# Kernel tuning notes

Measured on AMD Instinct MI355X. Metric: run time of the kernel, lower is better.

## Reference

```python
import jax, jax.numpy as jnp
import numpy as np

N = 100000     # nodes
E = 1600000    # edges
H = 64         # hidden_channels
FIN = 4        # input feature dim (GraphNorm(4))
EPS = 1e-5
STEPS = 3      # Set2Set processing steps


def setup_inputs() -> dict:
    key = jax.random.key(0)
    ks = jax.random.split(key, 20)
    rn = lambda k, shape, s=1.0: jax.random.normal(k, shape, dtype=jnp.float32) * s

    def gn_params(k, d):
        k1, k2 = jax.random.split(k)
        return (1.0 + 0.1 * rn(k1, (d,)), 0.1 * rn(k2, (d,)), jnp.ones((d,), jnp.float32))

    inp = {}
    inp['x'] = rn(ks[0], (N, FIN))
    inp['gn0_w'], inp['gn0_b'], inp['gn0_ms'] = gn_params(ks[1], FIN)
    inp['W1'] = rn(ks[2], (FIN, H), 1.0 / np.sqrt(FIN))
    inp['b1'] = 0.01 * rn(ks[3], (H,))
    inp['a1'] = 0.25 * jnp.ones((H,), jnp.float32)
    inp['gn1_w'], inp['gn1_b'], inp['gn1_ms'] = gn_params(ks[4], H)
    inp['W2'] = rn(ks[5], (H, H), 1.0 / np.sqrt(H))
    inp['b2'] = 0.01 * rn(ks[6], (H,))
    inp['a2'] = 0.25 * jnp.ones((H,), jnp.float32)
    inp['gn2_w'], inp['gn2_b'], inp['gn2_ms'] = gn_params(ks[7], H)
    inp['W3'] = rn(ks[8], (H, H), 1.0 / np.sqrt(H))
    inp['b3'] = 0.01 * rn(ks[9], (H,))
    inp['gn3_w'], inp['gn3_b'], inp['gn3_ms'] = gn_params(ks[10], H)
    s = 1.0 / np.sqrt(H)
    inp['Wih'] = rn(ks[11], (4 * H, 2 * H), s)  # LSTM input weights, gate order i,f,g,o
    inp['Whh'] = rn(ks[12], (4 * H, H), s)
    inp['bih'] = rn(ks[13], (4 * H,), s)
    inp['bhh'] = rn(ks[14], (4 * H,), s)
    inp['edge_index'] = jax.random.randint(ks[15], (2, E), 0, N, dtype=jnp.int32)
    return inp


def _graph_norm(x, w, b, ms):
    # single graph (batch all zeros): per-feature mean/var over all nodes
    mean = x.mean(0)
    out = x - ms * mean
    var = (out * out).mean(0)
    return w * out / jnp.sqrt(var + EPS) + b


def _prelu(x, a):
    return jnp.where(x >= 0, x, a * x)


def _gcn(x, W, b, src, dst, dinv):
    # GCNConv: D^{-1/2} (A + I) D^{-1/2} X W + b
    xw = x @ W
    coef = dinv[src] * dinv[dst]
    agg = jax.ops.segment_sum(xw[src] * coef[:, None], dst, num_segments=N)
    agg = agg + xw * (dinv * dinv)[:, None]  # self-loop contribution
    return agg + b


def reference(x, gn0_w, gn0_b, gn0_ms, W1, b1, a1, gn1_w, gn1_b, gn1_ms,
              W2, b2, a2, gn2_w, gn2_b, gn2_ms, W3, b3, gn3_w, gn3_b, gn3_ms,
              Wih, Whh, bih, bhh, edge_index):
    src, dst = edge_index[0], edge_index[1]
    deg = jax.ops.segment_sum(jnp.ones((E,), jnp.float32), dst, num_segments=N) + 1.0
    dinv = 1.0 / jnp.sqrt(deg)

    h = _graph_norm(x, gn0_w, gn0_b, gn0_ms)
    h = _prelu(_gcn(h, W1, b1, src, dst, dinv), a1)
    h = _graph_norm(h, gn1_w, gn1_b, gn1_ms)
    h = _prelu(_gcn(h, W2, b2, src, dst, dinv), a2)
    h = _graph_norm(h, gn2_w, gn2_b, gn2_ms)
    h = _gcn(h, W3, b3, src, dst, dinv)
    h = _graph_norm(h, gn3_w, gn3_b, gn3_ms)

    # Set2Set pooling over a single graph (batch forced to zeros in forward)
    q_star = jnp.zeros((1, 2 * H), jnp.float32)
    hs = jnp.zeros((1, H), jnp.float32)
    c = jnp.zeros((1, H), jnp.float32)
    for _ in range(STEPS):
        gates = q_star @ Wih.T + bih + hs @ Whh.T + bhh
        i, f, g, o = jnp.split(gates, 4, axis=-1)
        c = jax.nn.sigmoid(f) * c + jax.nn.sigmoid(i) * jnp.tanh(g)
        hs = jax.nn.sigmoid(o) * jnp.tanh(c)
        e = h @ hs[0]                    # [N] attention logits
        a = jax.nn.softmax(e)
        r = (a[:, None] * h).sum(0, keepdims=True)  # [1, H] readout
        q_star = jnp.concatenate([hs, r], axis=-1)
    return q_star  # [1, 2H]
```

## Files before the change

kernel.cpp:

```cpp
#include <hip/hip_runtime.h>

#define NN 100000
#define NE 1600000
#define HID 64
#define EPSV 1e-5f
#define NB_ATT 256

#define NBUK 391
#define BCAP 4608
#define BTILE 4096
#define NTILES 391

#define SM_SUMS(l)  ((l)*128)
#define SM_SUMSQ(l) ((l)*128 + 64)
#define SM_HS       512
#define SM_C        576
#define SM_HV       768
#define SM_EOFF     832
#define SM_COUNT    1024

#define NPAD        100352L
#define OFF_DINV    1024L
#define OFF_H       (OFF_DINV + NPAD)
#define OFF_Y32     (OFF_H + 6400000L)
#define OFF_PART    (OFF_Y32 + 3200000L)
#define OFF_INT     (OFF_PART + 69632L)

static __device__ __forceinline__ unsigned bf16rne(float f) {
  unsigned u = __float_as_uint(f);
  return (u + 0x7fffu + ((u >> 16) & 1u)) >> 16;
}
static __device__ __forceinline__ unsigned packbf2(float lo, float hi) {
  return bf16rne(lo) | (bf16rne(hi) << 16);
}
static __device__ __forceinline__ float bflo(unsigned w) { return __uint_as_float(w << 16); }
static __device__ __forceinline__ float bfhi(unsigned w) { return __uint_as_float(w & 0xffff0000u); }

static __device__ __forceinline__ void gn_affine(int j, const float* w, const float* b,
                                                 const float* ms, const float* sums,
                                                 const float* sumsq, float& sc, float& sh) {
  const float invn = 1.0f / (float)NN;
  float mean = sums[j] * invn;
  float ex2  = sumsq[j] * invn;
  float m    = ms[j];
  float var  = ex2 - m * mean * mean * (2.0f - m);
  sc = w[j] * rsqrtf(var + EPSV);
  sh = b[j] - sc * m * mean;
}

__global__ __launch_bounds__(512) void k_binit(int* __restrict__ gcursor) {
  int t = threadIdx.x;
  if (t < NBUK) gcursor[t] = t * BCAP;
}

__global__ __launch_bounds__(256) void k_bin(const int* __restrict__ src, const int* __restrict__ dst,
                                             int* __restrict__ gcursor, unsigned* __restrict__ stage) {
  __shared__ int hist[NBUK], base[NBUK];
  int t = threadIdx.x;
  long tile0 = (long)blockIdx.x * BTILE;
  for (int b = t; b < NBUK; b += 256) hist[b] = 0;
  __syncthreads();
  unsigned v[16]; int bk[16];
#pragma unroll
  for (int k = 0; k < 16; ++k) {
    long e = tile0 + k * 256 + t;
    if (e < NE) {
      int d = dst[e], s = src[e];
      bk[k] = d >> 8;
      v[k] = ((unsigned)(d & 255) << 24) | (unsigned)s;
      atomicAdd(&hist[bk[k]], 1);
    } else bk[k] = -1;
  }
  __syncthreads();
  for (int b = t; b < NBUK; b += 256) {
    int c = hist[b];
    base[b] = c ? atomicAdd(&gcursor[b], c) : 0;
    hist[b] = 0;
  }
  __syncthreads();
#pragma unroll
  for (int k = 0; k < 16; ++k) {
    if (bk[k] >= 0) {
      int off = atomicAdd(&hist[bk[k]], 1);
      stage[base[bk[k]] + off] = v[k];
    }
  }
}

__global__ __launch_bounds__(512) void k_bscan(const int* __restrict__ gcursor,
                                               int* __restrict__ boff, int* __restrict__ rowptr) {
  __shared__ int ws[8];
  int t = threadIdx.x, lane = t & 63;
  int c = (t < NBUK) ? (gcursor[t] - t * BCAP) : 0;
  int incl = c;
#pragma unroll
  for (int off = 1; off < 64; off <<= 1) {
    int u = __shfl_up(incl, off, 64);
    if (lane >= off) incl += u;
  }
  if (lane == 63) ws[t >> 6] = incl;
  __syncthreads();
  if (t == 0) {
    int s = 0;
#pragma unroll
    for (int w = 0; w < 8; ++w) { int tv = ws[w]; ws[w] = s; s += tv; }
  }
  __syncthreads();
  if (t < NBUK) boff[t] = incl - c + ws[t >> 6];
  if (t == 0) { boff[NBUK] = NE; rowptr[NN] = NE; }
}

__global__ __launch_bounds__(256) void k_bsort(const unsigned* __restrict__ stage,
                                               const int* __restrict__ boff,
                                               int* __restrict__ col, int* __restrict__ rowptr,
                                               float* __restrict__ dinv) {
  __shared__ int hist[256], cur[256];
  __shared__ int ws[4];
  int b = blockIdx.x;
  int t = threadIdx.x, lane = t & 63;
  int sb = b * BCAP;
  int b0 = boff[b], cb = boff[b + 1] - b0;
  hist[t] = 0;
  __syncthreads();
  for (int j = t; j < cb; j += 256)
    atomicAdd(&hist[stage[sb + j] >> 24], 1);
  __syncthreads();
  int c = hist[t];
  int incl = c;
#pragma unroll
  for (int off = 1; off < 64; off <<= 1) {
    int u = __shfl_up(incl, off, 64);
    if (lane >= off) incl += u;
  }
  if (lane == 63) ws[t >> 6] = incl;
  __syncthreads();
  int woff = 0;
  if (t >= 64) woff += ws[0];
  if (t >= 128) woff += ws[1];
  if (t >= 192) woff += ws[2];
  int gbase = b0 + (incl - c) + woff;
  int node = b * 256 + t;
  if (node < NN) {
    rowptr[node] = gbase;
    dinv[node] = rsqrtf((float)c + 1.0f);
  }
  cur[t] = gbase;
  __syncthreads();
  for (int j = t; j < cb; j += 256) {
    unsigned v = stage[sb + j];
    int pos = atomicAdd(&cur[v >> 24], 1);
    col[pos] = (int)(v & 0xffffffu);
  }
}

__global__ __launch_bounds__(256) void k_sums4(const float* __restrict__ x,
                                               float* __restrict__ sums, float* __restrict__ sumsq) {
  __shared__ float ls[256], lq[256];
  int t = threadIdx.x;
  float s = 0.f, q = 0.f;
  int stride = gridDim.x * blockDim.x;
  for (int idx = blockIdx.x * blockDim.x + t; idx < NN * 4; idx += stride) {
    float v = x[idx];
    s += v; q += v * v;
  }
  ls[t] = s; lq[t] = q;
  __syncthreads();
  if (t < 4) {
    float S = 0.f, Q = 0.f;
    for (int g = t; g < 256; g += 4) { S += ls[g]; Q += lq[g]; }
    atomicAdd(&sums[t], S);
    atomicAdd(&sumsq[t], Q);
  }
}

template <int D>
__global__ __launch_bounds__(256) void k_mm(const float* __restrict__ hin, const float* __restrict__ W,
                                            const float* __restrict__ gw, const float* __restrict__ gb,
                                            const float* __restrict__ gms,
                                            const float* __restrict__ sums, const float* __restrict__ sumsq,
                                            const float* __restrict__ dinv,
                                            unsigned* __restrict__ y32) {
  __shared__ float4 Ws4[D][16];
  __shared__ float4 woff4[16];
  __shared__ float scale[D], shift[D];
  __shared__ float hl[16][68];
  int t = threadIdx.x;
  if (t < D) {
    float sc, sh;
    gn_affine(t, gw, gb, gms, sums, sumsq, sc, sh);
    scale[t] = sc; shift[t] = sh;
  }
  __syncthreads();
  for (int idx = t; idx < D * 64; idx += 256) {
    int k = idx >> 6;
    ((float*)Ws4)[idx] = scale[k] * W[idx];
  }
  __syncthreads();
  if (t < 64) {
    float o = 0.f;
#pragma unroll
    for (int k = 0; k < D; ++k) o += shift[k] * W[k * 64 + t];
    ((float*)woff4)[t] = o;
  }
  __syncthreads();

  int row = t >> 4, cg = t & 15;
  const int nG = NN / 16;
  for (int g = blockIdx.x; g < nG; g += gridDim.x) {
    if (D == 64) {
      *(float4*)&hl[row][cg * 4] = *(const float4*)(hin + (long)(g * 16 + row) * 64 + cg * 4);
    } else {
      if (t < 64) hl[t >> 2][t & 3] = hin[g * 64 + t];
    }
    __syncthreads();
    float4 acc = woff4[cg];
#pragma unroll
    for (int k = 0; k < D; ++k) {
      float hk = hl[row][k];
      float4 w4 = Ws4[k][cg];
      acc.x += hk * w4.x; acc.y += hk * w4.y;
      acc.z += hk * w4.z; acc.w += hk * w4.w;
    }
    int node = g * 16 + row;
    float di = dinv[node];
    uint2 u;
    u.x = packbf2(di * acc.x, di * acc.y);
    u.y = packbf2(di * acc.z, di * acc.w);
    *(uint2*)(y32 + (long)node * 32 + 2 * cg) = u;
    __syncthreads();
  }
}

#define ACC4(W) { f[0]+=bflo(W.x); f[1]+=bfhi(W.x); f[2]+=bflo(W.y); f[3]+=bfhi(W.y); \
                  f[4]+=bflo(W.z); f[5]+=bfhi(W.z); f[6]+=bflo(W.w); f[7]+=bfhi(W.w); }

template <bool PR, bool HB>
__global__ __launch_bounds__(256) void k_gather_fin(const uint4* __restrict__ y4,
                                                    const int* __restrict__ rowptr, const int* __restrict__ col,
                                                    const float* __restrict__ dinv,
                                                    const float* __restrict__ b, const float* __restrict__ a,
                                                    float* __restrict__ h, uint4* __restrict__ hb4,
                                                    float* __restrict__ sums, float* __restrict__ sumsq) {
  __shared__ float lsum[4][64], lsq[4][64];
  int t = threadIdx.x, lane = t & 63, w = t >> 6;
  int o = lane >> 3, l7 = lane & 7;
  float bv[8], av[8];
#pragma unroll
  for (int k = 0; k < 8; ++k) {
    bv[k] = b[8 * l7 + k];
    av[k] = PR ? a[8 * l7 + k] : 1.f;
  }
  float sa[8] = {0,0,0,0,0,0,0,0}, qa[8] = {0,0,0,0,0,0,0,0};
  int nwaves = gridDim.x * 4;
  for (int i = blockIdx.x * 4 + w; i < NN; i += nwaves) {
    float f[8] = {0,0,0,0,0,0,0,0};
    int p = rowptr[i], p1 = rowptr[i + 1];
    for (; p + 16 <= p1; p += 16) {
      int c0 = col[p + o], c1 = col[p + 8 + o];
      uint4 wa = y4[c0 * 8 + l7];
      uint4 wb = y4[c1 * 8 + l7];
      ACC4(wa); ACC4(wb);
    }
    if (p + 8 <= p1) {
      int c0 = col[p + o];
      uint4 wa = y4[c0 * 8 + l7];
      ACC4(wa);
      p += 8;
    }
    {
      int r = p1 - p;
      int c = (o < r) ? col[p + o] : ((o == r) ? i : -1);
      if (c >= 0) {
        uint4 wa = y4[c * 8 + l7];
        ACC4(wa);
      }
    }
#pragma unroll
    for (int k = 0; k < 8; ++k) {
      float v = f[k];
      v += __shfl_xor(v, 8, 64);
      v += __shfl_xor(v, 16, 64);
      v += __shfl_xor(v, 32, 64);
      f[k] = v;
    }
    float di = dinv[i];
    float vo[8];
#pragma unroll
    for (int k = 0; k < 8; ++k) {
      float v = di * f[k] + bv[k];
      if (PR && v < 0.f) v *= av[k];
      vo[k] = v;
      sa[k] += v; qa[k] += v * v;
    }
    if (o == 0) {
      if (HB) {
        uint4 u;
        u.x = packbf2(vo[0], vo[1]); u.y = packbf2(vo[2], vo[3]);
        u.z = packbf2(vo[4], vo[5]); u.w = packbf2(vo[6], vo[7]);
        hb4[(long)i * 8 + l7] = u;
      } else {
        *(float4*)(h + (long)i * 64 + 8 * l7)     = make_float4(vo[0], vo[1], vo[2], vo[3]);
        *(float4*)(h + (long)i * 64 + 8 * l7 + 4) = make_float4(vo[4], vo[5], vo[6], vo[7]);
      }
    }
  }
  if (o == 0) {
#pragma unroll
    for (int k = 0; k < 8; ++k) { lsum[w][8 * l7 + k] = sa[k]; lsq[w][8 * l7 + k] = qa[k]; }
  }
  __syncthreads();
  if (t < 64) {
    float S = lsum[0][t] + lsum[1][t] + lsum[2][t] + lsum[3][t];
    float Q = lsq[0][t] + lsq[1][t] + lsq[2][t] + lsq[3][t];
    atomicAdd(&sums[t], S);
    atomicAdd(&sumsq[t], Q);
  }
}

__global__ __launch_bounds__(256) void k_att(const uint4* __restrict__ hb4, const float* __restrict__ sm,
                                             float* __restrict__ part) {
  __shared__ float gm[32], gz[32], gr[32][64];
  int t = threadIdx.x;
  int grp = t >> 3, l7 = t & 7;
  float hvr[8];
#pragma unroll
  for (int k = 0; k < 8; ++k) hvr[k] = sm[SM_HV + 8 * l7 + k];
  float eoff = sm[SM_EOFF];
  float m = -3.4e38f, z = 0.f;
  float r[8] = {0,0,0,0,0,0,0,0};
  int ngrp = gridDim.x * 32;
  for (int i = blockIdx.x * 32 + grp; i < NN; i += ngrp) {
    uint4 hw = hb4[(long)i * 8 + l7];
    float hx[8] = { bflo(hw.x), bfhi(hw.x), bflo(hw.y), bfhi(hw.y),
                    bflo(hw.z), bfhi(hw.z), bflo(hw.w), bfhi(hw.w) };
    float dot = 0.f;
#pragma unroll
    for (int k = 0; k < 8; ++k) dot += hx[k] * hvr[k];
    dot += __shfl_xor(dot, 1, 64);
    dot += __shfl_xor(dot, 2, 64);
    dot += __shfl_xor(dot, 4, 64);
    float e = dot + eoff;
    float mn = fmaxf(m, e);
    float sa = expf(m - mn);
    float pb = expf(e - mn);
    z = z * sa + pb;
#pragma unroll
    for (int k = 0; k < 8; ++k) r[k] = r[k] * sa + pb * hx[k];
    m = mn;
  }
#pragma unroll
  for (int k = 0; k < 8; ++k) gr[grp][8 * l7 + k] = r[k];
  if (l7 == 0) { gm[grp] = m; gz[grp] = z; }
  __syncthreads();
  if (t < 64) {
    float mb = gm[0];
#pragma unroll
    for (int k = 1; k < 32; ++k) mb = fmaxf(mb, gm[k]);
    float rb = 0.f, zb = 0.f;
#pragma unroll 8
    for (int k = 0; k < 32; ++k) {
      float scl = expf(gm[k] - mb);
      rb += gr[k][t] * scl;
      zb += gz[k] * scl;
    }
    part[blockIdx.x * 68 + t] = rb;
    if (t == 0) { part[blockIdx.x * 68 + 64] = mb; part[blockIdx.x * 68 + 65] = zb; }
  }
}

__global__ __launch_bounds__(256) void k_attfin(const float* __restrict__ part,
                                                const float* __restrict__ gw, const float* __restrict__ gb,
                                                const float* __restrict__ gms,
                                                const float* __restrict__ sums, const float* __restrict__ sumsq,
                                                const float* __restrict__ Wih, const float* __restrict__ Whh,
                                                const float* __restrict__ bih, const float* __restrict__ bhh,
                                                float* __restrict__ sm, float* __restrict__ out, int mode) {
  __shared__ float hsL[64], cL[64], qsL[128], gL[256], red[256], sf[NB_ATT], rr4[4][64];
  int t = threadIdx.x, lane = t & 63, w = t >> 6;
  if (t < 64) { hsL[t] = sm[SM_HS + t]; cL[t] = sm[SM_C + t]; }
  __syncthreads();
  if (mode > 0) {
    float mv = part[t * 68 + 64];
    red[t] = mv; __syncthreads();
    for (int s = 128; s; s >>= 1) { if (t < s) red[t] = fmaxf(red[t], red[t + s]); __syncthreads(); }
    float mg = red[0];
    __syncthreads();
    float sc_ = expf(mv - mg);
    sf[t] = sc_;
    red[t] = part[t * 68 + 65] * sc_; __syncthreads();
    for (int s = 128; s; s >>= 1) { if (t < s) red[t] += red[t + s]; __syncthreads(); }
    float zg = red[0];
    __syncthreads();
    float racc = 0.f;
#pragma unroll 8
    for (int j = 0; j < 64; ++j) {
      int bk = 4 * j + w;
      racc += part[bk * 68 + lane] * sf[bk];
    }
    rr4[w][lane] = racc;
    __syncthreads();
    if (t < 64) {
      float rg = rr4[0][t] + rr4[1][t] + rr4[2][t] + rr4[3][t];
      float sc, sh;
      gn_affine(t, gw, gb, gms, sums, sumsq, sc, sh);
      float rr = sc * (rg / zg) + sh;
      qsL[t] = hsL[t]; qsL[64 + t] = rr;
      if (mode == 2) { out[t] = hsL[t]; out[64 + t] = rr; }
    }
  } else {
    if (t < 64) { qsL[t] = 0.f; qsL[64 + t] = 0.f; hsL[t] = 0.f; cL[t] = 0.f; }
  }
  __syncthreads();
  if (mode == 2) return;
  float g = bih[t] + bhh[t];
#pragma unroll 16
  for (int k = 0; k < 128; ++k) g += qsL[k] * Wih[t * 128 + k];
#pragma unroll 16
  for (int k = 0; k < 64; ++k) g += hsL[k] * Whh[t * 64 + k];
  gL[t] = g;
  __syncthreads();
  if (t < 64) {
    float ig = 1.f / (1.f + expf(-gL[t]));
    float fg = 1.f / (1.f + expf(-gL[64 + t]));
    float gg = tanhf(gL[128 + t]);
    float og = 1.f / (1.f + expf(-gL[192 + t]));
    float c = fg * cL[t] + ig * gg;
    float hsn = og * tanhf(c);
    sm[SM_C + t] = c;
    sm[SM_HS + t] = hsn;
    float sc, sh;
    gn_affine(t, gw, gb, gms, sums, sumsq, sc, sh);
    sm[SM_HV + t] = sc * hsn;
    red[t] = sh * hsn;
  }
  __syncthreads();
  if (t == 0) {
    float s = 0.f;
    for (int k = 0; k < 64; ++k) s += red[k];
    sm[SM_EOFF] = s;
  }
}

extern "C" void kernel_launch(void* const* d_in, const int* in_sizes, int n_in,
                              void* d_out, int out_size, void* d_ws, size_t ws_size,
                              hipStream_t stream) {
  const float* x     = (const float*)d_in[0];
  const float* gn0_w = (const float*)d_in[1];
  const float* gn0_b = (const float*)d_in[2];
  const float* gn0_ms= (const float*)d_in[3];
  const float* W1    = (const float*)d_in[4];
  const float* b1    = (const float*)d_in[5];
  const float* a1    = (const float*)d_in[6];
  const float* gn1_w = (const float*)d_in[7];
  const float* gn1_b = (const float*)d_in[8];
  const float* gn1_ms= (const float*)d_in[9];
  const float* W2    = (const float*)d_in[10];
  const float* b2    = (const float*)d_in[11];
  const float* a2    = (const float*)d_in[12];
  const float* gn2_w = (const float*)d_in[13];
  const float* gn2_b = (const float*)d_in[14];
  const float* gn2_ms= (const float*)d_in[15];
  const float* W3    = (const float*)d_in[16];
  const float* b3    = (const float*)d_in[17];
  const float* gn3_w = (const float*)d_in[18];
  const float* gn3_b = (const float*)d_in[19];
  const float* gn3_ms= (const float*)d_in[20];
  const float* Wih   = (const float*)d_in[21];
  const float* Whh   = (const float*)d_in[22];
  const float* bih   = (const float*)d_in[23];
  const float* bhh   = (const float*)d_in[24];
  const int*   eidx  = (const int*)d_in[25];
  const int* esrc = eidx;
  const int* edst = eidx + NE;

  float* sm   = (float*)d_ws;
  float* dinv = sm + OFF_DINV;
  float* h    = sm + OFF_H;
  unsigned* stage = (unsigned*)(sm + OFF_H);
  uint4* hb4  = (uint4*)(sm + OFF_H);
  unsigned* y32 = (unsigned*)(sm + OFF_Y32);
  const uint4* y4 = (const uint4*)y32;
  float* part = sm + OFF_PART;
  int* col    = (int*)(sm + OFF_INT);
  int* rowptr = col + NE;
  int* gcursor= rowptr + NPAD;
  int* boff   = gcursor + 512;
  float* out  = (float*)d_out;

  hipMemsetAsync(sm, 0, SM_COUNT * sizeof(float), stream);

  k_binit<<<1, 512, 0, stream>>>(gcursor);
  k_bin<<<NTILES, 256, 0, stream>>>(esrc, edst, gcursor, stage);
  k_bscan<<<1, 512, 0, stream>>>(gcursor, boff, rowptr);
  k_bsort<<<NBUK, 256, 0, stream>>>(stage, boff, col, rowptr, dinv);

  k_sums4<<<1024, 256, 0, stream>>>(x, sm + SM_SUMS(0), sm + SM_SUMSQ(0));

  k_mm<4><<<1024, 256, 0, stream>>>(x, W1, gn0_w, gn0_b, gn0_ms,
                                    sm + SM_SUMS(0), sm + SM_SUMSQ(0), dinv, y32);
  k_gather_fin<true, false><<<2048, 256, 0, stream>>>(y4, rowptr, col, dinv, b1, a1, h, nullptr,
                                                      sm + SM_SUMS(1), sm + SM_SUMSQ(1));
  k_mm<64><<<1024, 256, 0, stream>>>(h, W2, gn1_w, gn1_b, gn1_ms,
                                     sm + SM_SUMS(1), sm + SM_SUMSQ(1), dinv, y32);
  k_gather_fin<true, false><<<2048, 256, 0, stream>>>(y4, rowptr, col, dinv, b2, a2, h, nullptr,
                                                      sm + SM_SUMS(2), sm + SM_SUMSQ(2));
  k_mm<64><<<1024, 256, 0, stream>>>(h, W3, gn2_w, gn2_b, gn2_ms,
                                     sm + SM_SUMS(2), sm + SM_SUMSQ(2), dinv, y32);
  k_gather_fin<false, true><<<2048, 256, 0, stream>>>(y4, rowptr, col, dinv, b3, nullptr, nullptr, hb4,
                                                      sm + SM_SUMS(3), sm + SM_SUMSQ(3));

  k_attfin<<<1, 256, 0, stream>>>(part, gn3_w, gn3_b, gn3_ms,
                                  sm + SM_SUMS(3), sm + SM_SUMSQ(3),
                                  Wih, Whh, bih, bhh, sm, nullptr, 0);
  for (int s = 0; s < 3; ++s) {
    k_att<<<NB_ATT, 256, 0, stream>>>(hb4, sm, part);
    k_attfin<<<1, 256, 0, stream>>>(part, gn3_w, gn3_b, gn3_ms,
                                    sm + SM_SUMS(3), sm + SM_SUMSQ(3),
                                    Wih, Whh, bih, bhh, sm,
                                    (s == 2) ? out : nullptr, (s == 2) ? 2 : 1);
  }
}
```

Measured before the change: 455.8 us.

## Fuse graph build and Set2Set tail into persistent kernels with grid barriers

Merges the binning, bucket scan, bucket sort and input-stat kernels into one persistent k_build kernel separated by software grid barriers, and merges the seven attention/LSTM tail launches into one k_tail kernel that also uses grid barriers. It also prefetches the next node's rowptr in the gather loop. The intent is to remove many small kernel launches and their gaps. The risk is that the spin barriers depend on all 784 or 256 blocks being resident at once, and that barrier latency may cost more than the launches it replaces.

```diff
diff --git a/kernel.cpp b/kernel.cpp
--- a/kernel.cpp
+++ b/kernel.cpp
@@ -8,8 +8,9 @@
 
 #define NBUK 391
 #define BCAP 4608
-#define BTILE 4096
-#define NTILES 391
+#define BTILE 2048
+#define NTILES 782
+#define NB_BUILD 784
 
 #define SM_SUMS(l)  ((l)*128)
 #define SM_SUMSQ(l) ((l)*128 + 64)
@@ -17,10 +18,12 @@
 #define SM_C        576
 #define SM_HV       768
 #define SM_EOFF     832
-#define SM_COUNT    1024
+#define SM_BAR      960
+#define SM_GCUR     1024
+#define SM_ZEND     1424
 
 #define NPAD        100352L
-#define OFF_DINV    1024L
+#define OFF_DINV    1424L
 #define OFF_H       (OFF_DINV + NPAD)
 #define OFF_Y32     (OFF_H + 6400000L)
 #define OFF_PART    (OFF_Y32 + 3200000L)
@@ -48,128 +51,156 @@
   sh = b[j] - sc * m * mean;
 }
 
-__global__ __launch_bounds__(512) void k_binit(int* __restrict__ gcursor) {
-  int t = threadIdx.x;
-  if (t < NBUK) gcursor[t] = t * BCAP;
-}
-
-__global__ __launch_bounds__(256) void k_bin(const int* __restrict__ src, const int* __restrict__ dst,
-                                             int* __restrict__ gcursor, unsigned* __restrict__ stage) {
+static __device__ __forceinline__ void gridbar(int* cnt, unsigned* flag, int nb) {
+  __syncthreads();
+  if (threadIdx.x == 0) {
+    __threadfence();
+    unsigned gen = atomicAdd(flag, 0u);
+    if (atomicAdd(cnt, 1) == nb - 1) {
+      atomicExch(cnt, 0);
+      __threadfence();
+      atomicAdd(flag, 1u);
+    } else {
+      while (atomicAdd(flag, 0u) == gen) __builtin_amdgcn_s_sleep(1);
+    }
+    __threadfence();
+  }
+  __syncthreads();
+}
+
+__global__ __launch_bounds__(256, 4) void k_build(const int* __restrict__ src, const int* __restrict__ dst,
+                                                  const float* __restrict__ x,
+                                                  int* __restrict__ gcursor, unsigned* __restrict__ stage,
+                                                  int* __restrict__ boff,
+                                                  int* __restrict__ col, int* __restrict__ rowptr,
+                                                  float* __restrict__ dinv,
+                                                  float* __restrict__ sums0, float* __restrict__ sumsq0,
+                                                  int* __restrict__ barc, unsigned* __restrict__ barf) {
   __shared__ int hist[NBUK], base[NBUK];
-  int t = threadIdx.x;
-  long tile0 = (long)blockIdx.x * BTILE;
-  for (int b = t; b < NBUK; b += 256) hist[b] = 0;
-  __syncthreads();
-  unsigned v[16]; int bk[16];
-#pragma unroll
-  for (int k = 0; k < 16; ++k) {
-    long e = tile0 + k * 256 + t;
-    if (e < NE) {
-      int d = dst[e], s = src[e];
-      bk[k] = d >> 8;
-      v[k] = ((unsigned)(d & 255) << 24) | (unsigned)s;
-      atomicAdd(&hist[bk[k]], 1);
-    } else bk[k] = -1;
-  }
-  __syncthreads();
-  for (int b = t; b < NBUK; b += 256) {
-    int c = hist[b];
-    base[b] = c ? atomicAdd(&gcursor[b], c) : 0;
-    hist[b] = 0;
-  }
-  __syncthreads();
-#pragma unroll
-  for (int k = 0; k < 16; ++k) {
-    if (bk[k] >= 0) {
-      int off = atomicAdd(&hist[bk[k]], 1);
-      stage[base[bk[k]] + off] = v[k];
-    }
-  }
-}
-
-__global__ __launch_bounds__(512) void k_bscan(const int* __restrict__ gcursor,
-                                               int* __restrict__ boff, int* __restrict__ rowptr) {
+  __shared__ int hist256[256], cur256[256];
   __shared__ int ws[8];
   int t = threadIdx.x, lane = t & 63;
-  int c = (t < NBUK) ? (gcursor[t] - t * BCAP) : 0;
-  int incl = c;
-#pragma unroll
-  for (int off = 1; off < 64; off <<= 1) {
-    int u = __shfl_up(incl, off, 64);
-    if (lane >= off) incl += u;
-  }
-  if (lane == 63) ws[t >> 6] = incl;
-  __syncthreads();
-  if (t == 0) {
-    int s = 0;
-#pragma unroll
-    for (int w = 0; w < 8; ++w) { int tv = ws[w]; ws[w] = s; s += tv; }
-  }
-  __syncthreads();
-  if (t < NBUK) boff[t] = incl - c + ws[t >> 6];
-  if (t == 0) { boff[NBUK] = NE; rowptr[NN] = NE; }
-}
-
-__global__ __launch_bounds__(256) void k_bsort(const unsigned* __restrict__ stage,
-                                               const int* __restrict__ boff,
-                                               int* __restrict__ col, int* __restrict__ rowptr,
-                                               float* __restrict__ dinv) {
-  __shared__ int hist[256], cur[256];
-  __shared__ int ws[4];
-  int b = blockIdx.x;
-  int t = threadIdx.x, lane = t & 63;
-  int sb = b * BCAP;
-  int b0 = boff[b], cb = boff[b + 1] - b0;
-  hist[t] = 0;
-  __syncthreads();
-  for (int j = t; j < cb; j += 256)
-    atomicAdd(&hist[stage[sb + j] >> 24], 1);
-  __syncthreads();
-  int c = hist[t];
-  int incl = c;
-#pragma unroll
-  for (int off = 1; off < 64; off <<= 1) {
-    int u = __shfl_up(incl, off, 64);
-    if (lane >= off) incl += u;
-  }
-  if (lane == 63) ws[t >> 6] = incl;
-  __syncthreads();
-  int woff = 0;
-  if (t >= 64) woff += ws[0];
-  if (t >= 128) woff += ws[1];
-  if (t >= 192) woff += ws[2];
-  int gbase = b0 + (incl - c) + woff;
-  int node = b * 256 + t;
-  if (node < NN) {
-    rowptr[node] = gbase;
-    dinv[node] = rsqrtf((float)c + 1.0f);
-  }
-  cur[t] = gbase;
-  __syncthreads();
-  for (int j = t; j < cb; j += 256) {
-    unsigned v = stage[sb + j];
-    int pos = atomicAdd(&cur[v >> 24], 1);
-    col[pos] = (int)(v & 0xffffffu);
-  }
-}
-
-__global__ __launch_bounds__(256) void k_sums4(const float* __restrict__ x,
-                                               float* __restrict__ sums, float* __restrict__ sumsq) {
-  __shared__ float ls[256], lq[256];
-  int t = threadIdx.x;
-  float s = 0.f, q = 0.f;
-  int stride = gridDim.x * blockDim.x;
-  for (int idx = blockIdx.x * blockDim.x + t; idx < NN * 4; idx += stride) {
-    float v = x[idx];
-    s += v; q += v * v;
-  }
-  ls[t] = s; lq[t] = q;
-  __syncthreads();
-  if (t < 4) {
-    float S = 0.f, Q = 0.f;
-    for (int g = t; g < 256; g += 4) { S += ls[g]; Q += lq[g]; }
-    atomicAdd(&sums[t], S);
-    atomicAdd(&sumsq[t], Q);
+
+  for (int tile = blockIdx.x; tile < NTILES; tile += gridDim.x) {
+    __syncthreads();
+    for (int b = t; b < NBUK; b += 256) hist[b] = 0;
+    __syncthreads();
+    long e0 = (long)tile * BTILE;
+    unsigned v[8]; int bk[8];
+#pragma unroll
+    for (int k = 0; k < 8; ++k) {
+      long e = e0 + k * 256 + t;
+      if (e < NE) {
+        int d = dst[e], s = src[e];
+        bk[k] = d >> 8;
+        v[k] = ((unsigned)(d & 255) << 24) | (unsigned)s;
+        atomicAdd(&hist[bk[k]], 1);
+      } else bk[k] = -1;
+    }
+    __syncthreads();
+    for (int b = t; b < NBUK; b += 256) {
+      int c = hist[b];
+      base[b] = c ? atomicAdd(&gcursor[b], c) : 0;
+      hist[b] = 0;
+    }
+    __syncthreads();
+#pragma unroll
+    for (int k = 0; k < 8; ++k) {
+      if (bk[k] >= 0) {
+        int bkk = bk[k];
+        int off = atomicAdd(&hist[bkk], 1);
+        stage[(long)bkk * BCAP + base[bkk] + off] = v[k];
+      }
+    }
+  }
+
+  {
+    const float4* x4 = (const float4*)x;
+    float4 s4 = make_float4(0.f, 0.f, 0.f, 0.f);
+    float4 q4 = make_float4(0.f, 0.f, 0.f, 0.f);
+    int stride = gridDim.x * 256;
+    for (int i = blockIdx.x * 256 + t; i < NN; i += stride) {
+      float4 xv = x4[i];
+      s4.x += xv.x; s4.y += xv.y; s4.z += xv.z; s4.w += xv.w;
+      q4.x += xv.x * xv.x; q4.y += xv.y * xv.y; q4.z += xv.z * xv.z; q4.w += xv.w * xv.w;
+    }
+#pragma unroll
+    for (int off = 32; off; off >>= 1) {
+      s4.x += __shfl_xor(s4.x, off, 64); s4.y += __shfl_xor(s4.y, off, 64);
+      s4.z += __shfl_xor(s4.z, off, 64); s4.w += __shfl_xor(s4.w, off, 64);
+      q4.x += __shfl_xor(q4.x, off, 64); q4.y += __shfl_xor(q4.y, off, 64);
+      q4.z += __shfl_xor(q4.z, off, 64); q4.w += __shfl_xor(q4.w, off, 64);
+    }
+    if (lane == 0) {
+      atomicAdd(&sums0[0], s4.x); atomicAdd(&sums0[1], s4.y);
+      atomicAdd(&sums0[2], s4.z); atomicAdd(&sums0[3], s4.w);
+      atomicAdd(&sumsq0[0], q4.x); atomicAdd(&sumsq0[1], q4.y);
+      atomicAdd(&sumsq0[2], q4.z); atomicAdd(&sumsq0[3], q4.w);
+    }
+  }
+
+  gridbar(barc, barf, gridDim.x);
+
+  if (blockIdx.x == 0) {
+    int t2 = 2 * t;
+    int c0 = (t2 < NBUK) ? gcursor[t2] : 0;
+    int c1 = (t2 + 1 < NBUK) ? gcursor[t2 + 1] : 0;
+    int ls = c0 + c1;
+    int incl = ls;
+#pragma unroll
+    for (int off = 1; off < 64; off <<= 1) {
+      int u = __shfl_up(incl, off, 64);
+      if (lane >= off) incl += u;
+    }
+    if (lane == 63) ws[t >> 6] = incl;
+    __syncthreads();
+    int woff = 0;
+    if (t >= 64) woff += ws[0];
+    if (t >= 128) woff += ws[1];
+    if (t >= 192) woff += ws[2];
+    int excl = incl - ls + woff;
+    if (t2 < NBUK) boff[t2] = excl;
+    if (t2 + 1 < NBUK) boff[t2 + 1] = excl + c0;
+    if (t == 0) { boff[NBUK] = NE; rowptr[NN] = NE; }
+  }
+
+  gridbar(barc, barf, gridDim.x);
+
+  for (int b = blockIdx.x; b < NBUK; b += gridDim.x) {
+    __syncthreads();
+    long sb = (long)b * BCAP;
+    int b0 = boff[b], cb = boff[b + 1] - b0;
+    hist256[t] = 0;
+    __syncthreads();
+    for (int j = t; j < cb; j += 256)
+      atomicAdd(&hist256[stage[sb + j] >> 24], 1);
+    __syncthreads();
+    int c = hist256[t];
+    int incl = c;
+#pragma unroll
+    for (int off = 1; off < 64; off <<= 1) {
+      int u = __shfl_up(incl, off, 64);
+      if (lane >= off) incl += u;
+    }
+    if (lane == 63) ws[t >> 6] = incl;
+    __syncthreads();
+    int woff = 0;
+    if (t >= 64) woff += ws[0];
+    if (t >= 128) woff += ws[1];
+    if (t >= 192) woff += ws[2];
+    int gbase = b0 + (incl - c) + woff;
+    int node = b * 256 + t;
+    if (node < NN) {
+      rowptr[node] = gbase;
+      dinv[node] = rsqrtf((float)c + 1.0f);
+    }
+    cur256[t] = gbase;
+    __syncthreads();
+    for (int j = t; j < cb; j += 256) {
+      unsigned v = stage[sb + j];
+      int pos = atomicAdd(&cur256[v >> 24], 1);
+      col[pos] = (int)(v & 0xffffffu);
+    }
   }
 }
 
@@ -252,9 +283,14 @@
   }
   float sa[8] = {0,0,0,0,0,0,0,0}, qa[8] = {0,0,0,0,0,0,0,0};
   int nwaves = gridDim.x * 4;
-  for (int i = blockIdx.x * 4 + w; i < NN; i += nwaves) {
+  int i = blockIdx.x * 4 + w;
+  int p = 0, p1 = 0;
+  if (i < NN) { p = rowptr[i]; p1 = rowptr[i + 1]; }
+  while (i < NN) {
+    int inext = i + nwaves;
+    int pn = 0, pn1 = 0;
+    if (inext < NN) { pn = rowptr[inext]; pn1 = rowptr[inext + 1]; }
     float f[8] = {0,0,0,0,0,0,0,0};
-    int p = rowptr[i], p1 = rowptr[i + 1];
     for (; p + 16 <= p1; p += 16) {
       int c0 = col[p + o], c1 = col[p + 8 + o];
       uint4 wa = y4[c0 * 8 + l7];
@@ -303,6 +339,7 @@
         *(float4*)(h + (long)i * 64 + 8 * l7 + 4) = make_float4(vo[4], vo[5], vo[6], vo[7]);
       }
     }
+    i = inext; p = pn; p1 = pn1;
   }
   if (o == 0) {
 #pragma unroll
@@ -317,9 +354,13 @@
   }
 }
 
-__global__ __launch_bounds__(256) void k_att(const uint4* __restrict__ hb4, const float* __restrict__ sm,
-                                             float* __restrict__ part) {
-  __shared__ float gm[32], gz[32], gr[32][64];
+struct TailSmem {
+  float gm[32], gz[32], gr[32][64];
+  float hsL[64], cL[64], qsL[128], gL[256], red[256], sf[NB_ATT], rr4[4][64];
+};
+
+static __device__ void att_phase(TailSmem& S, const uint4* __restrict__ hb4,
+                                 const float* __restrict__ sm, float* __restrict__ part) {
   int t = threadIdx.x;
   int grp = t >> 3, l7 = t & 7;
   float hvr[8];
@@ -341,103 +382,125 @@
     dot += __shfl_xor(dot, 4, 64);
     float e = dot + eoff;
     float mn = fmaxf(m, e);
-    float sa = expf(m - mn);
+    float sc = expf(m - mn);
     float pb = expf(e - mn);
-    z = z * sa + pb;
-#pragma unroll
-    for (int k = 0; k < 8; ++k) r[k] = r[k] * sa + pb * hx[k];
+    z = z * sc + pb;
+#pragma unroll
+    for (int k = 0; k < 8; ++k) r[k] = r[k] * sc + pb * hx[k];
     m = mn;
   }
 #pragma unroll
-  for (int k = 0; k < 8; ++k) gr[grp][8 * l7 + k] = r[k];
-  if (l7 == 0) { gm[grp] = m; gz[grp] = z; }
+  for (int k = 0; k < 8; ++k) S.gr[grp][8 * l7 + k] = r[k];
+  if (l7 == 0) { S.gm[grp] = m; S.gz[grp] = z; }
   __syncthreads();
   if (t < 64) {
-    float mb = gm[0];
-#pragma unroll
-    for (int k = 1; k < 32; ++k) mb = fmaxf(mb, gm[k]);
+    float mb = S.gm[0];
+#pragma unroll
+    for (int k = 1; k < 32; ++k) mb = fmaxf(mb, S.gm[k]);
     float rb = 0.f, zb = 0.f;
 #pragma unroll 8
     for (int k = 0; k < 32; ++k) {
-      float scl = expf(gm[k] - mb);
-      rb += gr[k][t] * scl;
-      zb += gz[k] * scl;
+      float scl = expf(S.gm[k] - mb);
+      rb += S.gr[k][t] * scl;
+      zb += S.gz[k] * scl;
     }
     part[blockIdx.x * 68 + t] = rb;
     if (t == 0) { part[blockIdx.x * 68 + 64] = mb; part[blockIdx.x * 68 + 65] = zb; }
   }
-}
-
-__global__ __launch_bounds__(256) void k_attfin(const float* __restrict__ part,
-                                                const float* __restrict__ gw, const float* __restrict__ gb,
-                                                const float* __restrict__ gms,
-                                                const float* __restrict__ sums, const float* __restrict__ sumsq,
-                                                const float* __restrict__ Wih, const float* __restrict__ Whh,
-                                                const float* __restrict__ bih, const float* __restrict__ bhh,
-                                                float* __restrict__ sm, float* __restrict__ out, int mode) {
-  __shared__ float hsL[64], cL[64], qsL[128], gL[256], red[256], sf[NB_ATT], rr4[4][64];
+  __syncthreads();
+}
+
+static __device__ void fin_phase(TailSmem& S, const float* __restrict__ part,
+                                 const float* __restrict__ gw, const float* __restrict__ gb,
+                                 const float* __restrict__ gms,
+                                 const float* __restrict__ sums, const float* __restrict__ sumsq,
+                                 const float* __restrict__ Wih, const float* __restrict__ Whh,
+                                 const float* __restrict__ bih, const float* __restrict__ bhh,
+                                 float* __restrict__ sm, float* __restrict__ out, int mode) {
   int t = threadIdx.x, lane = t & 63, w = t >> 6;
-  if (t < 64) { hsL[t] = sm[SM_HS + t]; cL[t] = sm[SM_C + t]; }
+  if (t < 64) { S.hsL[t] = sm[SM_HS + t]; S.cL[t] = sm[SM_C + t]; }
   __syncthreads();
   if (mode > 0) {
     float mv = part[t * 68 + 64];
-    red[t] = mv; __syncthreads();
-    for (int s = 128; s; s >>= 1) { if (t < s) red[t] = fmaxf(red[t], red[t + s]); __syncthreads(); }
-    float mg = red[0];
+    S.red[t] = mv; __syncthreads();
+    for (int s = 128; s; s >>= 1) { if (t < s) S.red[t] = fmaxf(S.red[t], S.red[t + s]); __syncthreads(); }
+    float mg = S.red[0];
     __syncthreads();
     float sc_ = expf(mv - mg);
-    sf[t] = sc_;
-    red[t] = part[t * 68 + 65] * sc_; __syncthreads();
-    for (int s = 128; s; s >>= 1) { if (t < s) red[t] += red[t + s]; __syncthreads(); }
-    float zg = red[0];
+    S.sf[t] = sc_;
+    S.red[t] = part[t * 68 + 65] * sc_; __syncthreads();
+    for (int s = 128; s; s >>= 1) { if (t < s) S.red[t] += S.red[t + s]; __syncthreads(); }
+    float zg = S.red[0];
     __syncthreads();
     float racc = 0.f;
 #pragma unroll 8
     for (int j = 0; j < 64; ++j) {
       int bk = 4 * j + w;
-      racc += part[bk * 68 + lane] * sf[bk];
-    }
-    rr4[w][lane] = racc;
+      racc += part[bk * 68 + lane] * S.sf[bk];
+    }
+    S.rr4[w][lane] = racc;
     __syncthreads();
     if (t < 64) {
-      float rg = rr4[0][t] + rr4[1][t] + rr4[2][t] + rr4[3][t];
+      float rg = S.rr4[0][t] + S.rr4[1][t] + S.rr4[2][t] + S.rr4[3][t];
       float sc, sh;
       gn_affine(t, gw, gb, gms, sums, sumsq, sc, sh);
       float rr = sc * (rg / zg) + sh;
-      qsL[t] = hsL[t]; qsL[64 + t] = rr;
-      if (mode == 2) { out[t] = hsL[t]; out[64 + t] = rr; }
+      S.qsL[t] = S.hsL[t]; S.qsL[64 + t] = rr;
+      if (mode == 2) { out[t] = S.hsL[t]; out[64 + t] = rr; }
     }
   } else {
-    if (t < 64) { qsL[t] = 0.f; qsL[64 + t] = 0.f; hsL[t] = 0.f; cL[t] = 0.f; }
+    if (t < 64) { S.qsL[t] = 0.f; S.qsL[64 + t] = 0.f; S.hsL[t] = 0.f; S.cL[t] = 0.f; }
   }
   __syncthreads();
   if (mode == 2) return;
   float g = bih[t] + bhh[t];
 #pragma unroll 16
-  for (int k = 0; k < 128; ++k) g += qsL[k] * Wih[t * 128 + k];
+  for (int k = 0; k < 128; ++k) g += S.qsL[k] * Wih[t * 128 + k];
 #pragma unroll 16
-  for (int k = 0; k < 64; ++k) g += hsL[k] * Whh[t * 64 + k];
-  gL[t] = g;
+  for (int k = 0; k < 64; ++k) g += S.hsL[k] * Whh[t * 64 + k];
+  S.gL[t] = g;
   __syncthreads();
   if (t < 64) {
-    float ig = 1.f / (1.f + expf(-gL[t]));
-    float fg = 1.f / (1.f + expf(-gL[64 + t]));
-    float gg = tanhf(gL[128 + t]);
-    float og = 1.f / (1.f + expf(-gL[192 + t]));
-    float c = fg * cL[t] + ig * gg;
+    float ig = 1.f / (1.f + expf(-S.gL[t]));
+    float fg = 1.f / (1.f + expf(-S.gL[64 + t]));
+    float gg = tanhf(S.gL[128 + t]);
+    float og = 1.f / (1.f + expf(-S.gL[192 + t]));
+    float c = fg * S.cL[t] + ig * gg;
     float hsn = og * tanhf(c);
     sm[SM_C + t] = c;
     sm[SM_HS + t] = hsn;
     float sc, sh;
     gn_affine(t, gw, gb, gms, sums, sumsq, sc, sh);
     sm[SM_HV + t] = sc * hsn;
-    red[t] = sh * hsn;
+    S.red[t] = sh * hsn;
   }
   __syncthreads();
   if (t == 0) {
     float s = 0.f;
-    for (int k = 0; k < 64; ++k) s += red[k];
+    for (int k = 0; k < 64; ++k) s += S.red[k];
     sm[SM_EOFF] = s;
+  }
+  __syncthreads();
+}
+
+__global__ __launch_bounds__(256) void k_tail(const uint4* __restrict__ hb4, float* __restrict__ part,
+                                              const float* __restrict__ gw, const float* __restrict__ gb,
+                                              const float* __restrict__ gms,
+                                              const float* __restrict__ sums, const float* __restrict__ sumsq,
+                                              const float* __restrict__ Wih, const float* __restrict__ Whh,
+                                              const float* __restrict__ bih, const float* __restrict__ bhh,
+                                              float* __restrict__ sm, float* __restrict__ out,
+                                              int* __restrict__ barc, unsigned* __restrict__ barf) {
+  __shared__ TailSmem S;
+  if (blockIdx.x == 0)
+    fin_phase(S, part, gw, gb, gms, sums, sumsq, Wih, Whh, bih, bhh, sm, nullptr, 0);
+  for (int s = 0; s < 3; ++s) {
+    gridbar(barc, barf, gridDim.x);
+    att_phase(S, hb4, sm, part);
+    gridbar(barc, barf, gridDim.x);
+    if (blockIdx.x == 0)
+      fin_phase(S, part, gw, gb, gms, sums, sumsq, Wih, Whh, bih, bhh, sm,
+                (s == 2) ? out : nullptr, (s == 2) ? 2 : 1);
   }
 }
 
@@ -474,6 +537,11 @@
   const int* edst = eidx + NE;
 
   float* sm   = (float*)d_ws;
+  int* gcursor= (int*)(sm + SM_GCUR);
+  int* barc   = (int*)(sm + SM_BAR);
+  unsigned* barf = (unsigned*)(sm + SM_BAR + 1);
+  int* barc2  = (int*)(sm + SM_BAR + 2);
+  unsigned* barf2 = (unsigned*)(sm + SM_BAR + 3);
   float* dinv = sm + OFF_DINV;
   float* h    = sm + OFF_H;
   unsigned* stage = (unsigned*)(sm + OFF_H);
@@ -483,18 +551,13 @@
   float* part = sm + OFF_PART;
   int* col    = (int*)(sm + OFF_INT);
   int* rowptr = col + NE;
-  int* gcursor= rowptr + NPAD;
-  int* boff   = gcursor + 512;
+  int* boff   = rowptr + NPAD;
   float* out  = (float*)d_out;
 
-  hipMemsetAsync(sm, 0, SM_COUNT * sizeof(float), stream);
-
-  k_binit<<<1, 512, 0, stream>>>(gcursor);
-  k_bin<<<NTILES, 256, 0, stream>>>(esrc, edst, gcursor, stage);
-  k_bscan<<<1, 512, 0, stream>>>(gcursor, boff, rowptr);
-  k_bsort<<<NBUK, 256, 0, stream>>>(stage, boff, col, rowptr, dinv);
-
-  k_sums4<<<1024, 256, 0, stream>>>(x, sm + SM_SUMS(0), sm + SM_SUMSQ(0));
+  hipMemsetAsync(sm, 0, SM_ZEND * sizeof(float), stream);
+
+  k_build<<<NB_BUILD, 256, 0, stream>>>(esrc, edst, x, gcursor, stage, boff, col, rowptr, dinv,
+                                        sm + SM_SUMS(0), sm + SM_SUMSQ(0), barc, barf);
 
   k_mm<4><<<1024, 256, 0, stream>>>(x, W1, gn0_w, gn0_b, gn0_ms,
                                     sm + SM_SUMS(0), sm + SM_SUMSQ(0), dinv, y32);
@@ -509,14 +572,7 @@
   k_gather_fin<false, true><<<2048, 256, 0, stream>>>(y4, rowptr, col, dinv, b3, nullptr, nullptr, hb4,
                                                       sm + SM_SUMS(3), sm + SM_SUMSQ(3));
 
-  k_attfin<<<1, 256, 0, stream>>>(part, gn3_w, gn3_b, gn3_ms,
-                                  sm + SM_SUMS(3), sm + SM_SUMSQ(3),
-                                  Wih, Whh, bih, bhh, sm, nullptr, 0);
-  for (int s = 0; s < 3; ++s) {
-    k_att<<<NB_ATT, 256, 0, stream>>>(hb4, sm, part);
-    k_attfin<<<1, 256, 0, stream>>>(part, gn3_w, gn3_b, gn3_ms,
-                                    sm + SM_SUMS(3), sm + SM_SUMSQ(3),
-                                    Wih, Whh, bih, bhh, sm,
-                                    (s == 2) ? out : nullptr, (s == 2) ? 2 : 1);
-  }
-}
+  k_tail<<<NB_ATT, 256, 0, stream>>>(hb4, part, gn3_w, gn3_b, gn3_ms,
+                                     sm + SM_SUMS(3), sm + SM_SUMSQ(3),
+                                     Wih, Whh, bih, bhh, sm, out, barc2, barf2);
+}
```

Result: slower. 846.6 us (+85.7%).

## Slice gather by feature chunk per block, fuse input stats into binning

Applied to the files above, without the earlier changes.

Each gather block now handles one 16-byte feature slice (blockIdx&7) across groups of 8 nodes, with 8 lanes striding edges per node. The intent is to shrink the per-pass working set of the gathered feature table so it fits better in cache. The x mean/variance reduction is folded into the binning kernel and the bucket-cursor init kernel is replaced by a memset, cutting two launches. Costs: rowptr and col are re-read by all 8 slices, and load balance is worse when node degrees vary.

```diff
diff --git a/kernel.cpp b/kernel.cpp
--- a/kernel.cpp
+++ b/kernel.cpp
@@ -5,6 +5,7 @@
 #define HID 64
 #define EPSV 1e-5f
 #define NB_ATT 256
+#define NGRP 12500
 
 #define NBUK 391
 #define BCAP 4608
@@ -17,10 +18,11 @@
 #define SM_C        576
 #define SM_HV       768
 #define SM_EOFF     832
-#define SM_COUNT    1024
+#define SM_GCUR     1024
+#define SM_ZEND     1424
 
 #define NPAD        100352L
-#define OFF_DINV    1024L
+#define OFF_DINV    1424L
 #define OFF_H       (OFF_DINV + NPAD)
 #define OFF_Y32     (OFF_H + 6400000L)
 #define OFF_PART    (OFF_Y32 + 3200000L)
@@ -48,15 +50,12 @@
   sh = b[j] - sc * m * mean;
 }
 
-__global__ __launch_bounds__(512) void k_binit(int* __restrict__ gcursor) {
-  int t = threadIdx.x;
-  if (t < NBUK) gcursor[t] = t * BCAP;
-}
-
 __global__ __launch_bounds__(256) void k_bin(const int* __restrict__ src, const int* __restrict__ dst,
-                                             int* __restrict__ gcursor, unsigned* __restrict__ stage) {
+                                             const float* __restrict__ x,
+                                             int* __restrict__ gcursor, unsigned* __restrict__ stage,
+                                             float* __restrict__ sums0, float* __restrict__ sumsq0) {
   __shared__ int hist[NBUK], base[NBUK];
-  int t = threadIdx.x;
+  int t = threadIdx.x, lane = t & 63;
   long tile0 = (long)blockIdx.x * BTILE;
   for (int b = t; b < NBUK; b += 256) hist[b] = 0;
   __syncthreads();
@@ -81,9 +80,32 @@
 #pragma unroll
   for (int k = 0; k < 16; ++k) {
     if (bk[k] >= 0) {
-      int off = atomicAdd(&hist[bk[k]], 1);
-      stage[base[bk[k]] + off] = v[k];
-    }
+      int bkk = bk[k];
+      int off = atomicAdd(&hist[bkk], 1);
+      stage[(long)bkk * BCAP + base[bkk] + off] = v[k];
+    }
+  }
+  const float4* x4 = (const float4*)x;
+  float4 s4 = make_float4(0.f, 0.f, 0.f, 0.f);
+  float4 q4 = make_float4(0.f, 0.f, 0.f, 0.f);
+  int stride = gridDim.x * 256;
+  for (int i = blockIdx.x * 256 + t; i < NN; i += stride) {
+    float4 xv = x4[i];
+    s4.x += xv.x; s4.y += xv.y; s4.z += xv.z; s4.w += xv.w;
+    q4.x += xv.x * xv.x; q4.y += xv.y * xv.y; q4.z += xv.z * xv.z; q4.w += xv.w * xv.w;
+  }
+#pragma unroll
+  for (int off = 32; off; off >>= 1) {
+    s4.x += __shfl_xor(s4.x, off, 64); s4.y += __shfl_xor(s4.y, off, 64);
+    s4.z += __shfl_xor(s4.z, off, 64); s4.w += __shfl_xor(s4.w, off, 64);
+    q4.x += __shfl_xor(q4.x, off, 64); q4.y += __shfl_xor(q4.y, off, 64);
+    q4.z += __shfl_xor(q4.z, off, 64); q4.w += __shfl_xor(q4.w, off, 64);
+  }
+  if (lane == 0) {
+    atomicAdd(&sums0[0], s4.x); atomicAdd(&sums0[1], s4.y);
+    atomicAdd(&sums0[2], s4.z); atomicAdd(&sums0[3], s4.w);
+    atomicAdd(&sumsq0[0], q4.x); atomicAdd(&sumsq0[1], q4.y);
+    atomicAdd(&sumsq0[2], q4.z); atomicAdd(&sumsq0[3], q4.w);
   }
 }
 
@@ -91,7 +113,7 @@
                                                int* __restrict__ boff, int* __restrict__ rowptr) {
   __shared__ int ws[8];
   int t = threadIdx.x, lane = t & 63;
-  int c = (t < NBUK) ? (gcursor[t] - t * BCAP) : 0;
+  int c = (t < NBUK) ? gcursor[t] : 0;
   int incl = c;
 #pragma unroll
   for (int off = 1; off < 64; off <<= 1) {
@@ -118,7 +140,7 @@
   __shared__ int ws[4];
   int b = blockIdx.x;
   int t = threadIdx.x, lane = t & 63;
-  int sb = b * BCAP;
+  long sb = (long)b * BCAP;
   int b0 = boff[b], cb = boff[b + 1] - b0;
   hist[t] = 0;
   __syncthreads();
@@ -150,26 +172,6 @@
     unsigned v = stage[sb + j];
     int pos = atomicAdd(&cur[v >> 24], 1);
     col[pos] = (int)(v & 0xffffffu);
-  }
-}
-
-__global__ __launch_bounds__(256) void k_sums4(const float* __restrict__ x,
-                                               float* __restrict__ sums, float* __restrict__ sumsq) {
-  __shared__ float ls[256], lq[256];
-  int t = threadIdx.x;
-  float s = 0.f, q = 0.f;
-  int stride = gridDim.x * blockDim.x;
-  for (int idx = blockIdx.x * blockDim.x + t; idx < NN * 4; idx += stride) {
-    float v = x[idx];
-    s += v; q += v * v;
-  }
-  ls[t] = s; lq[t] = q;
-  __syncthreads();
-  if (t < 4) {
-    float S = 0.f, Q = 0.f;
-    for (int g = t; g < 256; g += 4) { S += ls[g]; Q += lq[g]; }
-    atomicAdd(&sums[t], S);
-    atomicAdd(&sumsq[t], Q);
   }
 }
 
@@ -231,89 +233,83 @@
   }
 }
 
-#define ACC4(W) { f[0]+=bflo(W.x); f[1]+=bfhi(W.x); f[2]+=bflo(W.y); f[3]+=bfhi(W.y); \
-                  f[4]+=bflo(W.z); f[5]+=bfhi(W.z); f[6]+=bflo(W.w); f[7]+=bfhi(W.w); }
+#define ACCW(WV) { f[0]+=bflo(WV.x); f[1]+=bfhi(WV.x); f[2]+=bflo(WV.y); f[3]+=bfhi(WV.y); \
+                   f[4]+=bflo(WV.z); f[5]+=bfhi(WV.z); f[6]+=bflo(WV.w); f[7]+=bfhi(WV.w); }
 
 template <bool PR, bool HB>
-__global__ __launch_bounds__(256) void k_gather_fin(const uint4* __restrict__ y4,
+__global__ __launch_bounds__(256) void k_gather_fin(const uint4* __restrict__ y4x,
                                                     const int* __restrict__ rowptr, const int* __restrict__ col,
                                                     const float* __restrict__ dinv,
                                                     const float* __restrict__ b, const float* __restrict__ a,
                                                     float* __restrict__ h, uint4* __restrict__ hb4,
                                                     float* __restrict__ sums, float* __restrict__ sumsq) {
-  __shared__ float lsum[4][64], lsq[4][64];
+  __shared__ float ssum[8], ssq[8];
   int t = threadIdx.x, lane = t & 63, w = t >> 6;
-  int o = lane >> 3, l7 = lane & 7;
+  int n = lane >> 3, j = lane & 7;
+  int s = blockIdx.x & 7;
+  if (t < 8) { ssum[t] = 0.f; ssq[t] = 0.f; }
+  __syncthreads();
   float bv[8], av[8];
 #pragma unroll
   for (int k = 0; k < 8; ++k) {
-    bv[k] = b[8 * l7 + k];
-    av[k] = PR ? a[8 * l7 + k] : 1.f;
+    bv[k] = b[8 * s + k];
+    av[k] = PR ? a[8 * s + k] : 1.f;
   }
   float sa[8] = {0,0,0,0,0,0,0,0}, qa[8] = {0,0,0,0,0,0,0,0};
-  int nwaves = gridDim.x * 4;
-  for (int i = blockIdx.x * 4 + w; i < NN; i += nwaves) {
+  int gstride = (gridDim.x >> 3) * 4;
+  for (int g = (blockIdx.x >> 3) * 4 + w; g < NGRP; g += gstride) {
+    int i0 = g * 8;
+    int r = (lane < 9) ? rowptr[i0 + lane] : 0;
+    int p0 = __shfl(r, n, 64);
+    int p1 = __shfl(r, n + 1, 64);
     float f[8] = {0,0,0,0,0,0,0,0};
-    int p = rowptr[i], p1 = rowptr[i + 1];
-    for (; p + 16 <= p1; p += 16) {
-      int c0 = col[p + o], c1 = col[p + 8 + o];
-      uint4 wa = y4[c0 * 8 + l7];
-      uint4 wb = y4[c1 * 8 + l7];
-      ACC4(wa); ACC4(wb);
-    }
-    if (p + 8 <= p1) {
-      int c0 = col[p + o];
-      uint4 wa = y4[c0 * 8 + l7];
-      ACC4(wa);
-      p += 8;
-    }
-    {
-      int r = p1 - p;
-      int c = (o < r) ? col[p + o] : ((o == r) ? i : -1);
-      if (c >= 0) {
-        uint4 wa = y4[c * 8 + l7];
-        ACC4(wa);
-      }
+    for (int p = p0 + j; p < p1; p += 8) {
+      int c = col[p];
+      uint4 wv = y4x[(long)c * 8 + s];
+      ACCW(wv);
+    }
+    if (((p1 - p0) & 7) == j) {
+      uint4 wv = y4x[(long)(i0 + n) * 8 + s];
+      ACCW(wv);
     }
 #pragma unroll
     for (int k = 0; k < 8; ++k) {
       float v = f[k];
-      v += __shfl_xor(v, 8, 64);
-      v += __shfl_xor(v, 16, 64);
-      v += __shfl_xor(v, 32, 64);
+      v += __shfl_xor(v, 1, 64);
+      v += __shfl_xor(v, 2, 64);
+      v += __shfl_xor(v, 4, 64);
       f[k] = v;
     }
-    float di = dinv[i];
-    float vo[8];
-#pragma unroll
-    for (int k = 0; k < 8; ++k) {
-      float v = di * f[k] + bv[k];
-      if (PR && v < 0.f) v *= av[k];
-      vo[k] = v;
-      sa[k] += v; qa[k] += v * v;
-    }
-    if (o == 0) {
+    if (j == 0) {
+      int i = i0 + n;
+      float di = dinv[i];
+      float vo[8];
+#pragma unroll
+      for (int k = 0; k < 8; ++k) {
+        float v = di * f[k] + bv[k];
+        if (PR && v < 0.f) v *= av[k];
+        vo[k] = v;
+        sa[k] += v; qa[k] += v * v;
+      }
       if (HB) {
         uint4 u;
         u.x = packbf2(vo[0], vo[1]); u.y = packbf2(vo[2], vo[3]);
         u.z = packbf2(vo[4], vo[5]); u.w = packbf2(vo[6], vo[7]);
-        hb4[(long)i * 8 + l7] = u;
+        hb4[(long)i * 8 + s] = u;
       } else {
-        *(float4*)(h + (long)i * 64 + 8 * l7)     = make_float4(vo[0], vo[1], vo[2], vo[3]);
-        *(float4*)(h + (long)i * 64 + 8 * l7 + 4) = make_float4(vo[4], vo[5], vo[6], vo[7]);
+        *(float4*)(h + (long)i * 64 + 8 * s)     = make_float4(vo[0], vo[1], vo[2], vo[3]);
+        *(float4*)(h + (long)i * 64 + 8 * s + 4) = make_float4(vo[4], vo[5], vo[6], vo[7]);
       }
     }
   }
-  if (o == 0) {
-#pragma unroll
-    for (int k = 0; k < 8; ++k) { lsum[w][8 * l7 + k] = sa[k]; lsq[w][8 * l7 + k] = qa[k]; }
-  }
-  __syncthreads();
-  if (t < 64) {
-    float S = lsum[0][t] + lsum[1][t] + lsum[2][t] + lsum[3][t];
-    float Q = lsq[0][t] + lsq[1][t] + lsq[2][t] + lsq[3][t];
-    atomicAdd(&sums[t], S);
-    atomicAdd(&sumsq[t], Q);
+  if (j == 0) {
+#pragma unroll
+    for (int k = 0; k < 8; ++k) { atomicAdd(&ssum[k], sa[k]); atomicAdd(&ssq[k], qa[k]); }
+  }
+  __syncthreads();
+  if (t < 8) {
+    atomicAdd(&sums[8 * s + t], ssum[t]);
+    atomicAdd(&sumsq[8 * s + t], ssq[t]);
   }
 }
 
@@ -341,11 +337,11 @@
     dot += __shfl_xor(dot, 4, 64);
     float e = dot + eoff;
     float mn = fmaxf(m, e);
-    float sa = expf(m - mn);
+    float sc = expf(m - mn);
     float pb = expf(e - mn);
-    z = z * sa + pb;
-#pragma unroll
-    for (int k = 0; k < 8; ++k) r[k] = r[k] * sa + pb * hx[k];
+    z = z * sc + pb;
+#pragma unroll
+    for (int k = 0; k < 8; ++k) r[k] = r[k] * sc + pb * hx[k];
     m = mn;
   }
 #pragma unroll
@@ -393,8 +389,8 @@
     __syncthreads();
     float racc = 0.f;
 #pragma unroll 8
-    for (int j = 0; j < 64; ++j) {
-      int bk = 4 * j + w;
+    for (int jx = 0; jx < 64; ++jx) {
+      int bk = 4 * jx + w;
       racc += part[bk * 68 + lane] * sf[bk];
     }
     rr4[w][lane] = racc;
@@ -474,6 +470,7 @@
   const int* edst = eidx + NE;
 
   float* sm   = (float*)d_ws;
+  int* gcursor= (int*)(sm + SM_GCUR);
   float* dinv = sm + OFF_DINV;
   float* h    = sm + OFF_H;
   unsigned* stage = (unsigned*)(sm + OFF_H);
@@ -483,18 +480,15 @@
   float* part = sm + OFF_PART;
   int* col    = (int*)(sm + OFF_INT);
   int* rowptr = col + NE;
-  int* gcursor= rowptr + NPAD;
-  int* boff   = gcursor + 512;
+  int* boff   = rowptr + NPAD;
   float* out  = (float*)d_out;
 
-  hipMemsetAsync(sm, 0, SM_COUNT * sizeof(float), stream);
-
-  k_binit<<<1, 512, 0, stream>>>(gcursor);
-  k_bin<<<NTILES, 256, 0, stream>>>(esrc, edst, gcursor, stage);
+  hipMemsetAsync(sm, 0, SM_ZEND * sizeof(float), stream);
+
+  k_bin<<<NTILES, 256, 0, stream>>>(esrc, edst, x, gcursor, stage,
+                                    sm + SM_SUMS(0), sm + SM_SUMSQ(0));
   k_bscan<<<1, 512, 0, stream>>>(gcursor, boff, rowptr);
   k_bsort<<<NBUK, 256, 0, stream>>>(stage, boff, col, rowptr, dinv);
-
-  k_sums4<<<1024, 256, 0, stream>>>(x, sm + SM_SUMS(0), sm + SM_SUMSQ(0));
 
   k_mm<4><<<1024, 256, 0, stream>>>(x, W1, gn0_w, gn0_b, gn0_ms,
                                     sm + SM_SUMS(0), sm + SM_SUMSQ(0), dinv, y32);
```

Result: slower. 846.7 us (+85.7%).
